# Performance work log

Hardware: AMD Instinct MI355X
Metric: run time of the kernel (lower is better)

The kernel has to match this reference:

```python
import jax, jax.numpy as jnp
import numpy as np

# dims mirroring the torch module: dim=32 (MVN), omega=8, d_head=n_embd//n_head
B, T, E, DH = 8, 2048, 1024, 32
OMEGA, DIM = 8, 32
M = OMEGA * DIM  # 256 random features (omega concatenated N(0, I_dim) samples)


def setup_inputs() -> dict:
    key = jax.random.key(0)
    ks = jax.random.split(key, 8)
    s = 1.0 / np.sqrt(E).astype(np.float32)  # torch Linear-like init scale
    return {
        "x": jax.random.normal(ks[0], (B, T, E), jnp.float32),
        "Wq": jax.random.normal(ks[1], (E, DH), jnp.float32) * s,
        "bq": jax.random.normal(ks[2], (DH,), jnp.float32) * s,
        "Wk": jax.random.normal(ks[3], (E, DH), jnp.float32) * s,
        "bk": jax.random.normal(ks[4], (DH,), jnp.float32) * s,
        "Wv": jax.random.normal(ks[5], (E, DH), jnp.float32) * s,
        "bv": jax.random.normal(ks[6], (DH,), jnp.float32) * s,
        # random-feature matrix: omega stacked samples from N(0, I_DIM) -> [M, DH]
        "w": jax.random.normal(ks[7], (M, DH), jnp.float32),
    }


def reference(x, Wq, bq, Wk, bk, Wv, bv, w):
    # projections (as in Head.forward)
    q = x @ Wq + bq  # [B,T,DH]
    k = x @ Wk + bk  # [B,T,DH]
    v = x @ Wv + bv  # computed but unused, exactly as in the source
    del v
    # Aprox_softmax (FAVOR+-style hyperbolic random features), vectorized per token
    z = k + q                                          # [B,T,DH]
    zsqr = jnp.sum(k * k, -1) + jnp.sum(q * q, -1)     # [B,T]  (per-token norms)
    A = jnp.exp(-0.5 * zsqr)                           # [B,T]
    cosH = jnp.cosh(jnp.einsum('btd,md->btm', z, w))   # [B,T,M]
    R = A[..., None] * cosH                            # [B,T,M]
    return R
```

## Files before the change

### kernel.cpp

```cpp
#include <hip/hip_runtime.h>
#include <cstdint>

#define E_DIM   1024
#define DH      32
#define M_FEAT  256
#define BT      16384

typedef __attribute__((ext_vector_type(8))) short bf16x8;
typedef __attribute__((ext_vector_type(4))) float f32x4;

#define WP_H_OFF 0
#define WP_L_OFF 65536

__device__ __forceinline__ unsigned perm_hi2(unsigned lo_src, unsigned hi_src) {
#if __has_builtin(__builtin_amdgcn_perm)
    return __builtin_amdgcn_perm(hi_src, lo_src, 0x07060302u);
#else
    return (lo_src >> 16) | (hi_src & 0xFFFF0000u);
#endif
}

__device__ __forceinline__ void split2(float f0, float f1, unsigned& ph, unsigned& pl) {
    unsigned u0 = __builtin_bit_cast(unsigned, f0);
    unsigned u1 = __builtin_bit_cast(unsigned, f1);
    ph = perm_hi2(u0, u1);
    float d0 = f0 - __builtin_bit_cast(float, u0 & 0xFFFF0000u);
    float d1 = f1 - __builtin_bit_cast(float, u1 & 0xFFFF0000u);
    pl = perm_hi2(__builtin_bit_cast(unsigned, d0), __builtin_bit_cast(unsigned, d1));
}

__device__ __forceinline__ void split8(const float4& a, const float4& b,
                                       uint4& uh, uint4& ul) {
    split2(a.x, a.y, uh.x, ul.x);
    split2(a.z, a.w, uh.y, ul.y);
    split2(b.x, b.y, uh.z, ul.z);
    split2(b.z, b.w, uh.w, ul.w);
}

__global__ __launch_bounds__(256) void k_prep(
    const float* __restrict__ Wq, const float* __restrict__ Wk,
    short* __restrict__ ws)
{
    __shared__ float wlds[128 * 36];
    const int b = blockIdx.x, tid = threadIdx.x;
    const float* __restrict__ src = (b < 8) ? Wq : Wk;
    const int k0 = (b & 7) * 128;
    const int nbase = (b < 8) ? 0 : 32;
#pragma unroll
    for (int it = 0; it < 4; ++it) {
        int f = it * 256 + tid;
        int k = f >> 3, c4 = f & 7;
        float4 v = *(const float4*)(src + (size_t)(k0 + k) * DH + c4 * 4);
        *(float4*)&wlds[k * 36 + c4 * 4] = v;
    }
    __syncthreads();
    const int n = tid >> 3, kq = tid & 7;
    const int n_g = nbase + n;
    const int nt = n_g >> 4, ln = n_g & 15;
#pragma unroll
    for (int rep = 0; rep < 4; ++rep) {
        int kk = rep * 8 + kq;
        int k_g = k0 + kk * 4;
        float f0 = wlds[(kk * 4 + 0) * 36 + n];
        float f1 = wlds[(kk * 4 + 1) * 36 + n];
        float f2 = wlds[(kk * 4 + 2) * 36 + n];
        float f3 = wlds[(kk * 4 + 3) * 36 + n];
        uint2 ph, pl;
        split2(f0, f1, ph.x, pl.x);
        split2(f2, f3, ph.y, pl.y);
        int sub = k_g >> 5;
        int g = (k_g >> 3) & 3, j0 = k_g & 7;
        int lane = g * 16 + ln;
        size_t flat = ((size_t)(nt * 32 + sub)) * 512 + lane * 8 + j0;
        *(uint2*)(ws + WP_H_OFF + flat) = ph;
        *(uint2*)(ws + WP_L_OFF + flat) = pl;
    }
}

#define TB 16
#define XS2 136
#define QS 68
#define ZS 40

__global__ __launch_bounds__(256, 4) void k_main(
    const float* __restrict__ x, const float* __restrict__ bq,
    const float* __restrict__ bk, const short* __restrict__ ws,
    const float* __restrict__ w, float* __restrict__ out)
{
    __shared__ __align__(16) short xh_s[2][TB * XS2];
    __shared__ __align__(16) short xl_s[2][TB * XS2];
    __shared__ __align__(16) float qk_f[TB * QS];
    __shared__ __align__(16) short zh_s[TB * ZS];
    __shared__ __align__(16) short zl_s[TB * ZS];
    __shared__ float lnA_f[TB];

    const int tid  = threadIdx.x;
    const int lane = tid & 63;
    const int wv   = __builtin_amdgcn_readfirstlane(tid >> 6);
    const int ln15 = lane & 15;
    const int g    = lane >> 4;
    const long t0  = (long)blockIdx.x * TB;

    const int nrow = wv * 16 + ln15;
    const float bias = (nrow < 32) ? bq[nrow] : bk[nrow - 32];

    const int kq = tid & 15;
    const int mr = tid >> 4;

    f32x4 acc = {0.f, 0.f, 0.f, 0.f};

    const short* wpB_h = ws + WP_H_OFF + (size_t)(wv * 32) * 512 + lane * 8;
    const short* wpB_l = ws + WP_L_OFF + (size_t)(wv * 32) * 512 + lane * 8;
    const float* xrow  = x + (t0 + mr) * E_DIM + kq * 8;

    float4 sa = *(const float4*)(xrow + 0);
    float4 sb = *(const float4*)(xrow + 4);
    bf16x8 bcur_h[4], bcur_l[4], bnxt_h[4], bnxt_l[4];
#pragma unroll
    for (int j = 0; j < 4; ++j) {
        bcur_h[j] = *(const bf16x8*)(wpB_h + (size_t)j * 512);
        bcur_l[j] = *(const bf16x8*)(wpB_l + (size_t)j * 512);
    }
    {
        uint4 uh, ul;
        split8(sa, sb, uh, ul);
        *(uint4*)&xh_s[0][mr * XS2 + kq * 8] = uh;
        *(uint4*)&xl_s[0][mr * XS2 + kq * 8] = ul;
    }

#pragma unroll
    for (int p = 0; p < 8; ++p) {
        __syncthreads();
        if (p < 7) {
            sa = *(const float4*)(xrow + (p + 1) * 128);
            sb = *(const float4*)(xrow + (p + 1) * 128 + 4);
#pragma unroll
            for (int j = 0; j < 4; ++j) {
                bnxt_h[j] = *(const bf16x8*)(wpB_h + (size_t)((p + 1) * 4 + j) * 512);
                bnxt_l[j] = *(const bf16x8*)(wpB_l + (size_t)((p + 1) * 4 + j) * 512);
            }
        }
#pragma unroll
        for (int j = 0; j < 4; ++j) {
            bf16x8 ah = *(const bf16x8*)&xh_s[p & 1][ln15 * XS2 + j * 32 + g * 8];
            bf16x8 al = *(const bf16x8*)&xl_s[p & 1][ln15 * XS2 + j * 32 + g * 8];
            acc = __builtin_amdgcn_mfma_f32_16x16x32_bf16(ah, bcur_h[j], acc, 0, 0, 0);
            acc = __builtin_amdgcn_mfma_f32_16x16x32_bf16(ah, bcur_l[j], acc, 0, 0, 0);
            acc = __builtin_amdgcn_mfma_f32_16x16x32_bf16(al, bcur_h[j], acc, 0, 0, 0);
        }
        if (p < 7) {
            uint4 uh, ul;
            split8(sa, sb, uh, ul);
            *(uint4*)&xh_s[(p + 1) & 1][mr * XS2 + kq * 8] = uh;
            *(uint4*)&xl_s[(p + 1) & 1][mr * XS2 + kq * 8] = ul;
#pragma unroll
            for (int j = 0; j < 4; ++j) {
                bcur_h[j] = bnxt_h[j];
                bcur_l[j] = bnxt_l[j];
            }
        }
    }

    float4 wfa[4], wfb[4];
#pragma unroll
    for (int i = 0; i < 4; ++i) {
        const int nf = (wv * 4 + i) * 16 + ln15;
        wfa[i] = *(const float4*)(w + (size_t)nf * DH + g * 8);
        wfb[i] = *(const float4*)(w + (size_t)nf * DH + g * 8 + 4);
    }

#pragma unroll
    for (int r = 0; r < 4; ++r)
        qk_f[(g * 4 + r) * QS + nrow] = acc[r] + bias;
    __syncthreads();

    if (tid < 128) {
        const int tok = tid >> 3, grp = tid & 7;
        float4 qv = *(const float4*)&qk_f[tok * QS + grp * 4];
        float4 kv = *(const float4*)&qk_f[tok * QS + 32 + grp * 4];
        float z0 = qv.x + kv.x, z1 = qv.y + kv.y, z2 = qv.z + kv.z, z3 = qv.w + kv.w;
        float p = qv.x*qv.x + qv.y*qv.y + qv.z*qv.z + qv.w*qv.w
                + kv.x*kv.x + kv.y*kv.y + kv.z*kv.z + kv.w*kv.w;
        uint2 ph, pl;
        split2(z0, z1, ph.x, pl.x);
        split2(z2, z3, ph.y, pl.y);
        *(uint2*)&zh_s[tok * ZS + grp * 4] = ph;
        *(uint2*)&zl_s[tok * ZS + grp * 4] = pl;
        p += __shfl_xor(p, 1);
        p += __shfl_xor(p, 2);
        p += __shfl_xor(p, 4);
        if (grp == 0) lnA_f[tok] = -0.5f * p;
    }
    __syncthreads();

    f32x4 facc[4];
#pragma unroll
    for (int i = 0; i < 4; ++i) facc[i] = (f32x4){0.f,0.f,0.f,0.f};

    bf16x8 a_h = *(const bf16x8*)&zh_s[ln15 * ZS + g * 8];
    bf16x8 a_l = *(const bf16x8*)&zl_s[ln15 * ZS + g * 8];
#pragma unroll
    for (int i = 0; i < 4; ++i) {
        uint4 uh, ul;
        split8(wfa[i], wfb[i], uh, ul);
        bf16x8 bh = __builtin_bit_cast(bf16x8, uh);
        bf16x8 bl = __builtin_bit_cast(bf16x8, ul);
        facc[i] = __builtin_amdgcn_mfma_f32_16x16x32_bf16(a_h, bh, facc[i], 0, 0, 0);
        facc[i] = __builtin_amdgcn_mfma_f32_16x16x32_bf16(a_h, bl, facc[i], 0, 0, 0);
        facc[i] = __builtin_amdgcn_mfma_f32_16x16x32_bf16(a_l, bh, facc[i], 0, 0, 0);
    }

    float lnAv[4];
#pragma unroll
    for (int r = 0; r < 4; ++r) lnAv[r] = lnA_f[g * 4 + r];

#pragma unroll
    for (int i = 0; i < 4; ++i) {
        const int n = (wv * 4 + i) * 16 + ln15;
#pragma unroll
        for (int r = 0; r < 4; ++r) {
            float s = facc[i][r];
            float R = 0.5f * (__expf(lnAv[r] + s) + __expf(lnAv[r] - s));
            out[(t0 + g * 4 + r) * M_FEAT + n] = R;
        }
    }
}

extern "C" void kernel_launch(void* const* d_in, const int* in_sizes, int n_in,
                              void* d_out, int out_size, void* d_ws, size_t ws_size,
                              hipStream_t stream) {
    const float* x  = (const float*)d_in[0];
    const float* Wq = (const float*)d_in[1];
    const float* bq = (const float*)d_in[2];
    const float* Wk = (const float*)d_in[3];
    const float* bk = (const float*)d_in[4];
    const float* w  = (const float*)d_in[7];
    float* out = (float*)d_out;
    short* ws  = (short*)d_ws;

    k_prep<<<dim3(16), dim3(256), 0, stream>>>(Wq, Wk, ws);
    k_main<<<dim3(BT / TB), dim3(256), 0, stream>>>(x, bq, bk, ws, w, out);
}
```

Measured before the change: 123.3 us.

## Feed MFMA A-operands straight from global memory, dropping LDS staging of x

The projection loop no longer stages split bf16 hi/lo copies of x through double-buffered shared memory with a barrier per K-chunk. Each wave now loads its x fragment from global memory into registers, splits it locally, and runs two interleaved accumulators with a two-deep register prefetch. The weight-prep kernel is also rewritten as a direct per-thread gather with no shared memory, launched on more blocks. This removes LDS traffic and barriers from the main loop, but all four waves of a block now load and split the same x rows, so global/L1 traffic and VALU split work grow fourfold.

```diff
diff --git a/kernel.cpp b/kernel.cpp
--- a/kernel.cpp
+++ b/kernel.cpp
@@ -41,44 +41,26 @@
     const float* __restrict__ Wq, const float* __restrict__ Wk,
     short* __restrict__ ws)
 {
-    __shared__ float wlds[128 * 36];
-    const int b = blockIdx.x, tid = threadIdx.x;
-    const float* __restrict__ src = (b < 8) ? Wq : Wk;
-    const int k0 = (b & 7) * 128;
-    const int nbase = (b < 8) ? 0 : 32;
-#pragma unroll
-    for (int it = 0; it < 4; ++it) {
-        int f = it * 256 + tid;
-        int k = f >> 3, c4 = f & 7;
-        float4 v = *(const float4*)(src + (size_t)(k0 + k) * DH + c4 * 4);
-        *(float4*)&wlds[k * 36 + c4 * 4] = v;
-    }
-    __syncthreads();
-    const int n = tid >> 3, kq = tid & 7;
-    const int n_g = nbase + n;
-    const int nt = n_g >> 4, ln = n_g & 15;
-#pragma unroll
-    for (int rep = 0; rep < 4; ++rep) {
-        int kk = rep * 8 + kq;
-        int k_g = k0 + kk * 4;
-        float f0 = wlds[(kk * 4 + 0) * 36 + n];
-        float f1 = wlds[(kk * 4 + 1) * 36 + n];
-        float f2 = wlds[(kk * 4 + 2) * 36 + n];
-        float f3 = wlds[(kk * 4 + 3) * 36 + n];
-        uint2 ph, pl;
-        split2(f0, f1, ph.x, pl.x);
-        split2(f2, f3, ph.y, pl.y);
-        int sub = k_g >> 5;
-        int g = (k_g >> 3) & 3, j0 = k_g & 7;
-        int lane = g * 16 + ln;
-        size_t flat = ((size_t)(nt * 32 + sub)) * 512 + lane * 8 + j0;
-        *(uint2*)(ws + WP_H_OFF + flat) = ph;
-        *(uint2*)(ws + WP_L_OFF + flat) = pl;
-    }
+    const int idx  = blockIdx.x * 256 + threadIdx.x;
+    const int lane = idx & 63;
+    const int sub  = (idx >> 6) & 31;
+    const int nt   = idx >> 11;
+    const int n    = nt * 16 + (lane & 15);
+    const int kb   = sub * 32 + (lane >> 4) * 8;
+    const float* __restrict__ src = (n < 32) ? (Wq + n) : (Wk + n - 32);
+    float f[8];
+#pragma unroll
+    for (int j = 0; j < 8; ++j) f[j] = src[(size_t)(kb + j) * DH];
+    uint4 uh, ul;
+    split2(f[0], f[1], uh.x, ul.x);
+    split2(f[2], f[3], uh.y, ul.y);
+    split2(f[4], f[5], uh.z, ul.z);
+    split2(f[6], f[7], uh.w, ul.w);
+    *(uint4*)(ws + WP_H_OFF + (size_t)idx * 8) = uh;
+    *(uint4*)(ws + WP_L_OFF + (size_t)idx * 8) = ul;
 }
 
 #define TB 16
-#define XS2 136
 #define QS 68
 #define ZS 40
 
@@ -87,8 +69,6 @@
     const float* __restrict__ bk, const short* __restrict__ ws,
     const float* __restrict__ w, float* __restrict__ out)
 {
-    __shared__ __align__(16) short xh_s[2][TB * XS2];
-    __shared__ __align__(16) short xl_s[2][TB * XS2];
     __shared__ __align__(16) float qk_f[TB * QS];
     __shared__ __align__(16) short zh_s[TB * ZS];
     __shared__ __align__(16) short zl_s[TB * ZS];
@@ -104,62 +84,43 @@
     const int nrow = wv * 16 + ln15;
     const float bias = (nrow < 32) ? bq[nrow] : bk[nrow - 32];
 
-    const int kq = tid & 15;
-    const int mr = tid >> 4;
-
-    f32x4 acc = {0.f, 0.f, 0.f, 0.f};
-
-    const short* wpB_h = ws + WP_H_OFF + (size_t)(wv * 32) * 512 + lane * 8;
-    const short* wpB_l = ws + WP_L_OFF + (size_t)(wv * 32) * 512 + lane * 8;
-    const float* xrow  = x + (t0 + mr) * E_DIM + kq * 8;
-
-    float4 sa = *(const float4*)(xrow + 0);
-    float4 sb = *(const float4*)(xrow + 4);
-    bf16x8 bcur_h[4], bcur_l[4], bnxt_h[4], bnxt_l[4];
-#pragma unroll
-    for (int j = 0; j < 4; ++j) {
-        bcur_h[j] = *(const bf16x8*)(wpB_h + (size_t)j * 512);
-        bcur_l[j] = *(const bf16x8*)(wpB_l + (size_t)j * 512);
-    }
-    {
+    const float* xb  = x + (t0 + ln15) * (size_t)E_DIM + g * 8;
+    const short* wsh = ws + WP_H_OFF + (size_t)(wv * 32) * 512 + lane * 8;
+    const short* wsl = ws + WP_L_OFF + (size_t)(wv * 32) * 512 + lane * 8;
+
+    f32x4 acc[2] = {{0.f,0.f,0.f,0.f}, {0.f,0.f,0.f,0.f}};
+    float4 fxa[2], fxb[2];
+    bf16x8 bh[2], bl[2];
+
+#pragma unroll
+    for (int n = 0; n < 2; ++n) {
+        fxa[n] = *(const float4*)(xb + n * 32);
+        fxb[n] = *(const float4*)(xb + n * 32 + 4);
+        bh[n]  = *(const bf16x8*)(wsh + (size_t)n * 512);
+        bl[n]  = *(const bf16x8*)(wsl + (size_t)n * 512);
+    }
+
+#pragma unroll
+    for (int n = 0; n < 32; ++n) {
+        const int s = n & 1;
         uint4 uh, ul;
-        split8(sa, sb, uh, ul);
-        *(uint4*)&xh_s[0][mr * XS2 + kq * 8] = uh;
-        *(uint4*)&xl_s[0][mr * XS2 + kq * 8] = ul;
-    }
-
-#pragma unroll
-    for (int p = 0; p < 8; ++p) {
-        __syncthreads();
-        if (p < 7) {
-            sa = *(const float4*)(xrow + (p + 1) * 128);
-            sb = *(const float4*)(xrow + (p + 1) * 128 + 4);
-#pragma unroll
-            for (int j = 0; j < 4; ++j) {
-                bnxt_h[j] = *(const bf16x8*)(wpB_h + (size_t)((p + 1) * 4 + j) * 512);
-                bnxt_l[j] = *(const bf16x8*)(wpB_l + (size_t)((p + 1) * 4 + j) * 512);
-            }
+        split8(fxa[s], fxb[s], uh, ul);
+        bf16x8 ah = __builtin_bit_cast(bf16x8, uh);
+        bf16x8 al = __builtin_bit_cast(bf16x8, ul);
+        acc[s] = __builtin_amdgcn_mfma_f32_16x16x32_bf16(ah, bh[s], acc[s], 0, 0, 0);
+        acc[s] = __builtin_amdgcn_mfma_f32_16x16x32_bf16(ah, bl[s], acc[s], 0, 0, 0);
+        acc[s] = __builtin_amdgcn_mfma_f32_16x16x32_bf16(al, bh[s], acc[s], 0, 0, 0);
+        if (n < 30) {
+            fxa[s] = *(const float4*)(xb + (n + 2) * 32);
+            fxb[s] = *(const float4*)(xb + (n + 2) * 32 + 4);
+            bh[s]  = *(const bf16x8*)(wsh + (size_t)(n + 2) * 512);
+            bl[s]  = *(const bf16x8*)(wsl + (size_t)(n + 2) * 512);
         }
-#pragma unroll
-        for (int j = 0; j < 4; ++j) {
-            bf16x8 ah = *(const bf16x8*)&xh_s[p & 1][ln15 * XS2 + j * 32 + g * 8];
-            bf16x8 al = *(const bf16x8*)&xl_s[p & 1][ln15 * XS2 + j * 32 + g * 8];
-            acc = __builtin_amdgcn_mfma_f32_16x16x32_bf16(ah, bcur_h[j], acc, 0, 0, 0);
-            acc = __builtin_amdgcn_mfma_f32_16x16x32_bf16(ah, bcur_l[j], acc, 0, 0, 0);
-            acc = __builtin_amdgcn_mfma_f32_16x16x32_bf16(al, bcur_h[j], acc, 0, 0, 0);
-        }
-        if (p < 7) {
-            uint4 uh, ul;
-            split8(sa, sb, uh, ul);
-            *(uint4*)&xh_s[(p + 1) & 1][mr * XS2 + kq * 8] = uh;
-            *(uint4*)&xl_s[(p + 1) & 1][mr * XS2 + kq * 8] = ul;
-#pragma unroll
-            for (int j = 0; j < 4; ++j) {
-                bcur_h[j] = bnxt_h[j];
-                bcur_l[j] = bnxt_l[j];
-            }
-        }
-    }
+    }
+
+    f32x4 accv;
+#pragma unroll
+    for (int r = 0; r < 4; ++r) accv[r] = acc[0][r] + acc[1][r] + bias;
 
     float4 wfa[4], wfb[4];
 #pragma unroll
@@ -171,7 +132,7 @@
 
 #pragma unroll
     for (int r = 0; r < 4; ++r)
-        qk_f[(g * 4 + r) * QS + nrow] = acc[r] + bias;
+        qk_f[(g * 4 + r) * QS + nrow] = accv[r];
     __syncthreads();
 
     if (tid < 128) {
@@ -203,11 +164,11 @@
     for (int i = 0; i < 4; ++i) {
         uint4 uh, ul;
         split8(wfa[i], wfb[i], uh, ul);
-        bf16x8 bh = __builtin_bit_cast(bf16x8, uh);
-        bf16x8 bl = __builtin_bit_cast(bf16x8, ul);
-        facc[i] = __builtin_amdgcn_mfma_f32_16x16x32_bf16(a_h, bh, facc[i], 0, 0, 0);
-        facc[i] = __builtin_amdgcn_mfma_f32_16x16x32_bf16(a_h, bl, facc[i], 0, 0, 0);
-        facc[i] = __builtin_amdgcn_mfma_f32_16x16x32_bf16(a_l, bh, facc[i], 0, 0, 0);
+        bf16x8 wh = __builtin_bit_cast(bf16x8, uh);
+        bf16x8 wl = __builtin_bit_cast(bf16x8, ul);
+        facc[i] = __builtin_amdgcn_mfma_f32_16x16x32_bf16(a_h, wh, facc[i], 0, 0, 0);
+        facc[i] = __builtin_amdgcn_mfma_f32_16x16x32_bf16(a_h, wl, facc[i], 0, 0, 0);
+        facc[i] = __builtin_amdgcn_mfma_f32_16x16x32_bf16(a_l, wh, facc[i], 0, 0, 0);
     }
 
     float lnAv[4];
@@ -238,6 +199,6 @@
     float* out = (float*)d_out;
     short* ws  = (short*)d_ws;
 
-    k_prep<<<dim3(16), dim3(256), 0, stream>>>(Wq, Wk, ws);
+    k_prep<<<dim3(32), dim3(256), 0, stream>>>(Wq, Wk, ws);
     k_main<<<dim3(BT / TB), dim3(256), 0, stream>>>(x, bq, bk, ws, w, out);
 }
```

Result: slower. 144.2 us (+16.9%).
